# Optimization experiments

Hardware: AMD Instinct MI355X
Metric: run time of the kernel (lower is better)

## Reference

```python
import jax, jax.numpy as jnp
import numpy as np
import math

HEADS = 2
DH = 64
INNER = HEADS * DH  # 128
TOPK = 128
ALPHA = 10.0
N_FREQ = 8  # feature_dim // (2*input_dim) = 64 // 8
OMEGAS = jnp.logspace(1.0, math.log10(128.0), N_FREQ)           # sigma_q = 128
OMEGAS_L = [jnp.logspace(1.0, math.log10(s), N_FREQ) for s in (128.0, 32.0)]
LAYER_NUM = 2


def calc_gamma(grid, omegas):
    # grid: (Q, 4) -> (Q, 4*2*n_freq)
    arg = jnp.pi * grid[:, :, None] * omegas[None, None, :]      # (Q,4,n)
    g = jnp.concatenate([jnp.sin(arg), jnp.cos(arg)], axis=-1)   # (Q,4,2n)
    return g.reshape(grid.shape[0], -1)


def setup_inputs() -> dict:
    key = jax.random.key(0)
    ks = jax.random.split(key, 20)
    B, Q, L, HD, FD, OD = 2, 4096, 1024, 256, 64, 1

    def w(k, shape, fan_in):
        return jax.random.normal(k, shape, dtype=jnp.float32) * (1.0 / np.sqrt(fan_in))

    inp = {
        'x': jax.random.uniform(ks[0], (B, Q, 4), dtype=jnp.float32),
        'tokens': jax.random.normal(ks[1], (B, L, HD), dtype=jnp.float32),
        'query_W': w(ks[2], (FD, HD), FD),
        'query_b': jnp.zeros((HD,), jnp.float32),
        'q_W': w(ks[3], (HD, INNER), HD),
        'kv_W': w(ks[4], (HD, 2 * INNER), HD),
        'out_W': w(ks[5], (INNER, HD), INNER),
        'out_b': jnp.zeros((HD,), jnp.float32),
        'band_W': w(ks[6], (LAYER_NUM, FD, HD), FD),
        'band_b': jnp.zeros((LAYER_NUM, HD), jnp.float32),
        'mod_W': w(ks[7], (LAYER_NUM, HD, HD), HD),
        'mod_b': jnp.zeros((LAYER_NUM, HD), jnp.float32),
        'hv_W': w(ks[8], (LAYER_NUM - 1, HD, HD), HD),
        'hv_b': jnp.zeros((LAYER_NUM - 1, HD), jnp.float32),
        'outl_W': w(ks[9], (LAYER_NUM, HD, OD), HD),
        'outl_b': jnp.zeros((LAYER_NUM, OD), jnp.float32),
        'gD': 8, 'gH': 8, 'gW': 8, 'gT': 8,
    }
    return inp


def reference(x, tokens, query_W, query_b, q_W, kv_W, out_W, out_b,
              band_W, band_b, mod_W, mod_b, hv_W, hv_b, outl_W, outl_b,
              gD, gH, gW, gT):
    B, Q, _ = x.shape
    L = tokens.shape[1]
    grid = x[0]  # (Q, 4) — torch code uses x[0] for all batches

    # --- patch index + approximate relative distances -> sparse attn indices ---
    z_i = (grid[:, 0] * gD).astype(jnp.int32)
    y_i = (grid[:, 1] * gH).astype(jnp.int32)
    x_i = (grid[:, 2] * gW).astype(jnp.int32)
    t_i = (grid[:, 3] * gT).astype(jnp.int32)
    idx = ((t_i * gD + z_i) * gH + y_i) * gW + x_i               # (Q,)
    N = gD * gH * gW * gT
    t = idx / N                                                  # (Q,) float
    tok_pos = (jnp.arange(L, dtype=jnp.float32) + 0.5) / L       # (L,)
    bias = ALPHA * (t[:, None] - tok_pos[None, :]) ** 2          # (Q, L)
    # top-k SMALLEST distances (identical across batch, compute once)
    _, attn_idx = jax.lax.top_k(-bias, TOPK)                     # (Q, k)

    # --- query features ---
    gamma_q = calc_gamma(grid, OMEGAS)                           # (Q, 64)
    x_q = jax.nn.relu(gamma_q @ query_W + query_b)               # (Q, 256)
    x_q = jnp.broadcast_to(x_q[None], (B, Q, x_q.shape[-1]))

    # --- sparse shared-token cross attention ---
    scale = DH ** -0.5
    q = (x_q @ q_W).reshape(B, Q, HEADS, DH)                     # (B,Q,H,Dh)
    kv = tokens @ kv_W                                           # (B,L,2*inner)
    k_full, v_full = kv[..., :INNER], kv[..., INNER:]            # (B,L,inner)
    k_sp = k_full[:, attn_idx, :].reshape(B, Q, TOPK, HEADS, DH)  # (B,Q,k,H,Dh)
    v_sp = v_full[:, attn_idx, :].reshape(B, Q, TOPK, HEADS, DH)
    sim = jnp.einsum('bqhd,bqkhd->bhqk', q, k_sp) * scale        # (B,H,Q,k)
    attn = jax.nn.softmax(sim, axis=-1)
    o = jnp.einsum('bhqk,bqkhd->bqhd', attn, v_sp).reshape(B, Q, INNER)
    modulation = o @ out_W + out_b                               # (B,Q,256)

    # --- per-band modulation ---
    mods = []
    for l in range(LAYER_NUM):
        gamma_l = calc_gamma(grid, OMEGAS_L[l])                  # (Q, 64)
        h_l = jax.nn.relu(gamma_l @ band_W[l] + band_b[l])       # (Q, 256)
        m_l = jax.nn.relu(h_l[None] + modulation @ mod_W[l] + mod_b[l])
        mods.append(m_l)

    h_v = [mods[0]]
    for i in range(LAYER_NUM - 1):
        h_v.append(jax.nn.relu((mods[i + 1] + h_v[i]) @ hv_W[i] + hv_b[i]))

    out = sum(h_v[i] @ outl_W[i] + outl_b[i] for i in range(LAYER_NUM))
    return out  # (B, Q, output_dim)
```

## Files before the change

kernel.cpp:

```cpp
#include <hip/hip_runtime.h>
#include <math.h>

#define BN     2
#define QN     4096
#define LN     1024
#define TOPKN  128
#define PI_F   3.14159265358979323846f

#define LOG2R0 0.52543879f
#define LOG2R1 0.23972456f

#define NCMAX  320
#define PFP    332

typedef __attribute__((ext_vector_type(8))) short  s16x8;
typedef __attribute__((ext_vector_type(4))) short  s16x4;
typedef __attribute__((ext_vector_type(4))) float  f32x4;
typedef unsigned short u16;

__device__ __forceinline__ u16 f2bf(float f) {
    unsigned int u = __float_as_uint(f);
    u = (u + 0x7FFFu + ((u >> 16) & 1u)) >> 16;
    return (u16)u;
}

__device__ __forceinline__ s16x8 ldB(const float* __restrict__ base, int stride) {
    s16x8 r;
    #pragma unroll
    for (int jj = 0; jj < 8; jj++) r[jj] = (short)f2bf(base[(size_t)jj * stride]);
    return r;
}

__device__ __forceinline__ size_t wtile(int n, int k, int K) {
    return (size_t)((n >> 4) * (K >> 5) + (k >> 5)) * 512 + (n & 15) * 32 + (k & 31);
}
__device__ __forceinline__ size_t kidx(int b, int l, int d) {
    return (((size_t)(b * 64 + (l >> 4)) * 16 + (d >> 3)) * 16 + (l & 15)) * 8 + (d & 7);
}
__device__ __forceinline__ size_t vidx(int b, int n, int k) {
    return (((size_t)(b * 8 + (n >> 4)) * 128 + (k >> 3)) * 16 + (n & 15)) * 8 + (k & 7);
}

struct KvS { u16 tok[32 * 264]; };
struct QS  { float shx[128]; u16 gam[32 * 72]; u16 xq[32 * 264]; };
struct TrS { float tile[8][32][33]; };
struct SoS { int hist[1024]; int cur[1024]; };
union PrepS { KvS kv; QS q; TrS tr; SoS so; };

__global__ __launch_bounds__(1024) void prep_kernel(
    const float* __restrict__ tokens, const float* __restrict__ kv_W,
    const float* __restrict__ x, const float* __restrict__ query_W,
    const float* __restrict__ query_b, const float* __restrict__ q_W,
    const float* __restrict__ outW, const float* __restrict__ bandW,
    const float* __restrict__ modW, const float* __restrict__ hvW,
    const int* __restrict__ gDp, const int* __restrict__ gHp,
    const int* __restrict__ gWp, const int* __restrict__ gTp,
    u16* __restrict__ qall, u16* __restrict__ kbf, u16* __restrict__ vtbf,
    u16* __restrict__ outT, u16* __restrict__ bandT,
    u16* __restrict__ modT, u16* __restrict__ hvT,
    int* __restrict__ perm, int* __restrict__ ssort)
{
    __shared__ __align__(16) PrepS sm;
    const int bid = blockIdx.x;
    const int t   = threadIdx.x;
    const int wid = t >> 6, lane = t & 63;
    const int quad = lane >> 4, l16 = lane & 15;

    if (bid < 64) {
        int l0 = bid * 32;
        int b = l0 >> 10, lloc = l0 & 1023;
        #pragma unroll
        for (int i = 0; i < 8; i++) {
            int idx = i * 1024 + t; int row = idx >> 8, col = idx & 255;
            sm.kv.tok[row * 264 + col] = f2bf(tokens[(size_t)(l0 + row) * 256 + col]);
        }
        __syncthreads();
        int m0 = (wid & 1) * 16;
        int c0 = (wid >> 1) * 32;
        f32x4 acc[2];
        acc[0] = (f32x4){0.f, 0.f, 0.f, 0.f};
        acc[1] = (f32x4){0.f, 0.f, 0.f, 0.f};
        for (int kc = 0; kc < 8; kc++) {
            s16x8 a = *(const s16x8*)&sm.kv.tok[(m0 + l16) * 264 + kc * 32 + quad * 8];
            #pragma unroll
            for (int sub = 0; sub < 2; sub++) {
                s16x8 bfr = ldB(&kv_W[(size_t)(kc * 32 + quad * 8) * 256 + c0 + sub * 16 + l16], 256);
                acc[sub] = __builtin_amdgcn_mfma_f32_16x16x32_bf16(a, bfr, acc[sub], 0, 0, 0);
            }
        }
        #pragma unroll
        for (int sub = 0; sub < 2; sub++) {
            int col = c0 + sub * 16 + l16;
            if (col < 128) {
                #pragma unroll
                for (int r = 0; r < 4; r++)
                    kbf[kidx(b, lloc + m0 + quad * 4 + r, col)] = f2bf(acc[sub][r]);
            } else {
                s16x4 pk;
                pk[0] = (short)f2bf(acc[sub][0]); pk[1] = (short)f2bf(acc[sub][1]);
                pk[2] = (short)f2bf(acc[sub][2]); pk[3] = (short)f2bf(acc[sub][3]);
                *(s16x4*)&vtbf[vidx(b, col - 128, lloc + m0 + quad * 4)] = pk;
            }
        }
    } else if (bid < 192) {
        int p0 = (bid - 64) * 32;
        if (t < 128) sm.q.shx[t] = x[p0 * 4 + t];
        __syncthreads();
        #pragma unroll
        for (int j = 0; j < 2; j++) {
            int e = t * 2 + j;
            int g = e >> 6, f = e & 63;
            int c = f >> 4, jj = f & 15, oi = jj & 7;
            float om = 10.0f * exp2f((float)oi * LOG2R0);
            float arg = PI_F * sm.q.shx[g * 4 + c] * om;
            sm.q.gam[g * 72 + f] = f2bf((jj < 8) ? __sinf(arg) : __cosf(arg));
        }
        __syncthreads();
        int m0 = (wid & 1) * 16;
        {
            int c0 = (wid >> 1) * 32;
            f32x4 acc[2];
            acc[0] = (f32x4){0.f, 0.f, 0.f, 0.f};
            acc[1] = (f32x4){0.f, 0.f, 0.f, 0.f};
            for (int kc = 0; kc < 2; kc++) {
                s16x8 a = *(const s16x8*)&sm.q.gam[(m0 + l16) * 72 + kc * 32 + quad * 8];
                #pragma unroll
                for (int sub = 0; sub < 2; sub++) {
                    s16x8 bfr = ldB(&query_W[(size_t)(kc * 32 + quad * 8) * 256 + c0 + sub * 16 + l16], 256);
                    acc[sub] = __builtin_amdgcn_mfma_f32_16x16x32_bf16(a, bfr, acc[sub], 0, 0, 0);
                }
            }
            #pragma unroll
            for (int sub = 0; sub < 2; sub++) {
                int col = c0 + sub * 16 + l16;
                float bias = query_b[col];
                #pragma unroll
                for (int r = 0; r < 4; r++)
                    sm.q.xq[(m0 + quad * 4 + r) * 264 + col] = f2bf(fmaxf(acc[sub][r] + bias, 0.f));
            }
        }
        __syncthreads();
        {
            int n0q = (wid >> 1) * 16;
            f32x4 acc2 = (f32x4){0.f, 0.f, 0.f, 0.f};
            for (int kc = 0; kc < 8; kc++) {
                s16x8 a = *(const s16x8*)&sm.q.xq[(m0 + l16) * 264 + kc * 32 + quad * 8];
                s16x8 bfr = ldB(&q_W[(size_t)(kc * 32 + quad * 8) * 128 + n0q + l16], 128);
                acc2 = __builtin_amdgcn_mfma_f32_16x16x32_bf16(a, bfr, acc2, 0, 0, 0);
            }
            #pragma unroll
            for (int r = 0; r < 4; r++)
                qall[(size_t)(p0 + m0 + quad * 4 + r) * 128 + n0q + l16] = f2bf(acc2[r]);
        }
    } else if (bid < 224) {
        int base = (bid - 192) * 8;
        int tx = t & 31, ty = (t >> 5) & 31;
        #pragma unroll
        for (int it = 0; it < 8; it++) {
            int lt_g = base + it;
            const float* src; int K, lt;
            if (lt_g < 32)       { src = outW;  K = 128; lt = lt_g; }
            else if (lt_g < 64)  { src = bandW; K = 128; lt = lt_g - 32; }
            else if (lt_g < 192) { src = modW;  K = 512; lt = lt_g - 64; }
            else                 { src = hvW;   K = 256; lt = lt_g - 192; }
            int tk = K >> 5;
            int k0 = (lt % tk) * 32, n0 = (lt / tk) * 32;
            sm.tr.tile[it][ty][tx] = src[(size_t)(k0 + ty) * 256 + n0 + tx];
        }
        __syncthreads();
        #pragma unroll
        for (int it = 0; it < 8; it++) {
            int lt_g = base + it;
            u16* dst; int K, lt;
            if (lt_g < 32)       { dst = outT;  K = 128; lt = lt_g; }
            else if (lt_g < 64)  { dst = bandT; K = 128; lt = lt_g - 32; }
            else if (lt_g < 192) { dst = modT;  K = 512; lt = lt_g - 64; }
            else                 { dst = hvT;   K = 256; lt = lt_g - 192; }
            int tk = K >> 5;
            int k0 = (lt % tk) * 32, n0 = (lt / tk) * 32;
            dst[wtile(n0 + ty, k0 + tx, K)] = f2bf(sm.tr.tile[it][tx][ty]);
        }
    } else {
        int gD = gDp[0], gH = gHp[0], gW = gWp[0], gT = gTp[0];
        int Ng = gD * gH * gW * gT;
        sm.so.hist[t] = 0;
        __syncthreads();
        int sarr[4];
        #pragma unroll
        for (int i = 0; i < 4; i++) {
            int q = i * 1024 + t;
            float4 xv = *(const float4*)&x[q * 4];
            int zi = (int)(xv.x * (float)gD);
            int yi = (int)(xv.y * (float)gH);
            int xi = (int)(xv.z * (float)gW);
            int ti = (int)(xv.w * (float)gT);
            int idx = ((ti * gD + zi) * gH + yi) * gW + xi;
            float tt = (float)idx / (float)Ng;
            int s = (int)ceilf(tt * (float)LN - ((float)(TOPKN / 2) + 0.5f));
            s = min(max(s, 0), LN - TOPKN);
            sarr[i] = s;
            atomicAdd(&sm.so.hist[s], 1);
        }
        __syncthreads();
        int cnt = sm.so.hist[t];
        int incl = cnt;
        #pragma unroll
        for (int off = 1; off < 64; off <<= 1) {
            int u = __shfl_up(incl, off);
            if (lane >= off) incl += u;
        }
        if (lane == 63) sm.so.cur[wid] = incl;
        __syncthreads();
        if (wid == 0) {
            int v = (lane < 16) ? sm.so.cur[lane] : 0;
            #pragma unroll
            for (int off = 1; off < 16; off <<= 1) {
                int u = __shfl_up(v, off);
                if (lane >= off) v += u;
            }
            if (lane < 16) sm.so.cur[lane] = v;
        }
        __syncthreads();
        int woff = wid ? sm.so.cur[wid - 1] : 0;
        sm.so.hist[t] = woff + incl - cnt;
        __syncthreads();
        #pragma unroll
        for (int i = 0; i < 4; i++) {
            int q = i * 1024 + t;
            int pos = atomicAdd(&sm.so.hist[sarr[i]], 1);
            perm[pos] = q;
            ssort[pos] = sarr[i];
        }
    }
}

__global__ __launch_bounds__(1024, 8) void fused_kernel(
    const float* __restrict__ x,
    const u16* __restrict__ kbf, const u16* __restrict__ vtbf,
    const u16* __restrict__ qall,
    const int* __restrict__ perm, const int* __restrict__ ssort,
    const u16* __restrict__ outT, const float* __restrict__ out_b,
    const u16* __restrict__ bandT, const float* __restrict__ band_b,
    const u16* __restrict__ modT, const float* __restrict__ mod_b,
    const u16* __restrict__ hvT, const float* __restrict__ hv_b,
    const float* __restrict__ outl_W, const float* __restrict__ outl_b,
    float* __restrict__ out)
{
    const int bid = blockIdx.x;
    const int b   = bid >> 8;
    const int sp0 = (bid & 255) * 16;
    const int t   = threadIdx.x;
    const int wid = t >> 6, lane = t & 63;
    const int quad = lane >> 4, l16 = lane & 15;

    __shared__ __align__(16) u16 q_bf[16 * 136];
    __shared__ __align__(16) u16 gam_lds[32 * 72];
    __shared__ __align__(16) float scores32[32 * PFP];
    __shared__ __align__(16) u16 o_lds[16 * 136];
    __shared__ float fin[256];
    __shared__ float sh_xc[64];
    __shared__ int sh_pq[16], sh_s[16];

    u16* modu_lds = (u16*)scores32;
    u16* s01_lds  = ((u16*)scores32) + 16 * 264;

    if (t < 16) { sh_pq[t] = perm[sp0 + t]; sh_s[t] = ssort[sp0 + t]; }
    __syncthreads();

    {
        int m = t >> 6, d = (t & 63) * 2;
        *(unsigned int*)&q_bf[m * 136 + d] =
            *(const unsigned int*)&qall[(size_t)sh_pq[m] * 128 + d];
    }
    if (t < 64) sh_xc[t] = x[(size_t)sh_pq[t >> 2] * 4 + (t & 3)];
    __syncthreads();

    #pragma unroll
    for (int j = 0; j < 2; j++) {
        int e = t * 2 + j;
        int l = e >> 10, g = (e >> 6) & 15, f = e & 63;
        int c = f >> 4, jj = f & 15, oi = jj & 7;
        float om = 10.0f * exp2f((float)oi * (l ? LOG2R1 : LOG2R0));
        float arg = PI_F * sh_xc[g * 4 + c] * om;
        gam_lds[(l * 16 + g) * 72 + f] = f2bf((jj < 8) ? __sinf(arg) : __cosf(arg));
    }

    const int u0    = sh_s[0] & ~15;
    const int ncols = min((sh_s[15] + 128 - u0 + 31) & ~31, NCMAX);
    const int nsub  = ncols >> 4;

    {
        s16x8 aq00 = *(const s16x8*)&q_bf[l16 * 136 + quad * 8];
        s16x8 aq01 = *(const s16x8*)&q_bf[l16 * 136 + 32 + quad * 8];
        s16x8 aq10 = *(const s16x8*)&q_bf[l16 * 136 + 64 + quad * 8];
        s16x8 aq11 = *(const s16x8*)&q_bf[l16 * 136 + 96 + quad * 8];
        for (int j = wid; j < 2 * nsub; j += 16) {
            int h = (j >= nsub) ? 1 : 0;
            int sub = j - h * nsub;
            int lrow = u0 + sub * 16 + l16;
            f32x4 acc = (f32x4){0.f, 0.f, 0.f, 0.f};
            s16x8 b0 = *(const s16x8*)&kbf[kidx(b, lrow, h * 64 + quad * 8)];
            s16x8 b1 = *(const s16x8*)&kbf[kidx(b, lrow, h * 64 + 32 + quad * 8)];
            acc = __builtin_amdgcn_mfma_f32_16x16x32_bf16(h ? aq10 : aq00, b0, acc, 0, 0, 0);
            acc = __builtin_amdgcn_mfma_f32_16x16x32_bf16(h ? aq11 : aq01, b1, acc, 0, 0, 0);
            #pragma unroll
            for (int r = 0; r < 4; r++)
                scores32[(h * 16 + quad * 4 + r) * PFP + sub * 16 + l16] = acc[r];
        }
    }
    __syncthreads();

    {
        int g = wid;
        int sg = sh_s[g];
        #pragma unroll
        for (int rr = 0; rr < 2; rr++) {
            int row = g + rr * 16;
            float vals[5]; int ok[5];
            float mx = -1e30f;
            #pragma unroll
            for (int i = 0; i < 5; i++) {
                int c = lane + 64 * i;
                float v = scores32[row * PFP + c] * 0.125f;
                int key = u0 + c;
                int o2 = (c < ncols) && (key >= sg) && (key < sg + 128);
                vals[i] = v; ok[i] = o2;
                if (o2) mx = fmaxf(mx, v);
            }
            #pragma unroll
            for (int off = 1; off < 64; off <<= 1) mx = fmaxf(mx, __shfl_xor(mx, off));
            float sum = 0.f, e5[5];
            #pragma unroll
            for (int i = 0; i < 5; i++) {
                float e = ok[i] ? __expf(vals[i] - mx) : 0.f;
                e5[i] = e; sum += e;
            }
            #pragma unroll
            for (int off = 1; off < 64; off <<= 1) sum += __shfl_xor(sum, off);
            float inv = 1.f / sum;
            u16* prow = (u16*)&scores32[row * PFP];
            #pragma unroll
            for (int i = 0; i < 5; i++) {
                int c = lane + 64 * i;
                prow[c] = f2bf(e5[i] * inv);
            }
        }
    }
    __syncthreads();

    if (wid < 8) {
        int n0 = wid * 16;
        int hh = n0 >> 6;
        const u16* prow = (const u16*)&scores32[(hh * 16 + l16) * PFP];
        f32x4 acc = (f32x4){0.f, 0.f, 0.f, 0.f};
        for (int kc = 0; kc < (NCMAX >> 5); kc++) {
            s16x8 a = *(const s16x8*)&prow[kc * 32 + quad * 8];
            int koff = u0 + kc * 32 + quad * 8;
            koff = min(koff, 1016);
            s16x8 bfr = *(const s16x8*)&vtbf[vidx(b, n0 + l16, koff)];
            acc = __builtin_amdgcn_mfma_f32_16x16x32_bf16(a, bfr, acc, 0, 0, 0);
        }
        #pragma unroll
        for (int r = 0; r < 4; r++)
            o_lds[(quad * 4 + r) * 136 + n0 + l16] = f2bf(acc[r]);
    }
    __syncthreads();

    const int n0 = wid * 16;
    float m0f[4];

    {
        f32x4 acc = (f32x4){0.f, 0.f, 0.f, 0.f};
        #pragma unroll
        for (int kc = 0; kc < 4; kc++) {
            s16x8 a = *(const s16x8*)&o_lds[l16 * 136 + kc * 32 + quad * 8];
            s16x8 bfr = *(const s16x8*)&outT[wtile(n0 + l16, kc * 32 + quad * 8, 128)];
            acc = __builtin_amdgcn_mfma_f32_16x16x32_bf16(a, bfr, acc, 0, 0, 0);
        }
        int col = n0 + l16;
        float bias = out_b[col];
        #pragma unroll
        for (int r = 0; r < 4; r++)
            modu_lds[(quad * 4 + r) * 264 + col] = f2bf(acc[r] + bias);
    }
    __syncthreads();

    #pragma unroll
    for (int l = 0; l < 2; l++) {
        f32x4 acc1 = (f32x4){0.f, 0.f, 0.f, 0.f};
        f32x4 acc2 = (f32x4){0.f, 0.f, 0.f, 0.f};
        #pragma unroll
        for (int kc = 0; kc < 2; kc++) {
            s16x8 a = *(const s16x8*)&gam_lds[(l * 16 + l16) * 72 + kc * 32 + quad * 8];
            s16x8 bfr = *(const s16x8*)&bandT[wtile(n0 + l16, l * 64 + kc * 32 + quad * 8, 128)];
            acc1 = __builtin_amdgcn_mfma_f32_16x16x32_bf16(a, bfr, acc1, 0, 0, 0);
        }
        #pragma unroll
        for (int kc = 0; kc < 8; kc++) {
            s16x8 a = *(const s16x8*)&modu_lds[l16 * 264 + kc * 32 + quad * 8];
            s16x8 bfr = *(const s16x8*)&modT[wtile(n0 + l16, l * 256 + kc * 32 + quad * 8, 512)];
            acc2 = __builtin_amdgcn_mfma_f32_16x16x32_bf16(a, bfr, acc2, 0, 0, 0);
        }
        int col = n0 + l16;
        float bb = band_b[l * 256 + col];
        float mb = mod_b[l * 256 + col];
        #pragma unroll
        for (int r = 0; r < 4; r++) {
            float hval = fmaxf(acc1[r] + bb, 0.f);
            float mval = fmaxf(hval + acc2[r] + mb, 0.f);
            if (l == 0) m0f[r] = mval;
            else s01_lds[(quad * 4 + r) * 264 + col] = f2bf(m0f[r] + mval);
        }
    }
    __syncthreads();

    {
        f32x4 acc = (f32x4){0.f, 0.f, 0.f, 0.f};
        #pragma unroll
        for (int kc = 0; kc < 8; kc++) {
            s16x8 a = *(const s16x8*)&s01_lds[l16 * 264 + kc * 32 + quad * 8];
            s16x8 bfr = *(const s16x8*)&hvT[wtile(n0 + l16, kc * 32 + quad * 8, 256)];
            acc = __builtin_amdgcn_mfma_f32_16x16x32_bf16(a, bfr, acc, 0, 0, 0);
        }
        int col = n0 + l16;
        float w0 = outl_W[col], w1 = outl_W[256 + col], hb = hv_b[col];
        #pragma unroll
        for (int r = 0; r < 4; r++) {
            float hvv = fmaxf(acc[r] + hb, 0.f);
            float pv = m0f[r] * w0 + hvv * w1;
            #pragma unroll
            for (int off = 1; off < 16; off <<= 1) pv += __shfl_xor(pv, off);
            if (l16 == 0) fin[wid * 16 + quad * 4 + r] = pv;
        }
    }
    __syncthreads();
    if (t < 16) {
        float s2 = outl_b[0] + outl_b[1];
        #pragma unroll
        for (int w = 0; w < 16; w++) s2 += fin[w * 16 + t];
        out[(size_t)b * QN + sh_pq[t]] = s2;
    }
}

extern "C" void kernel_launch(void* const* d_in, const int* in_sizes, int n_in,
                              void* d_out, int out_size, void* d_ws, size_t ws_size,
                              hipStream_t stream)
{
    const float* x       = (const float*)d_in[0];
    const float* tokens  = (const float*)d_in[1];
    const float* query_W = (const float*)d_in[2];
    const float* query_b = (const float*)d_in[3];
    const float* q_W     = (const float*)d_in[4];
    const float* kv_W    = (const float*)d_in[5];
    const float* out_W   = (const float*)d_in[6];
    const float* out_b   = (const float*)d_in[7];
    const float* band_W  = (const float*)d_in[8];
    const float* band_b  = (const float*)d_in[9];
    const float* mod_W   = (const float*)d_in[10];
    const float* mod_b   = (const float*)d_in[11];
    const float* hv_W    = (const float*)d_in[12];
    const float* hv_b    = (const float*)d_in[13];
    const float* outl_W  = (const float*)d_in[14];
    const float* outl_b  = (const float*)d_in[15];
    const int*   gD      = (const int*)d_in[16];
    const int*   gH      = (const int*)d_in[17];
    const int*   gW      = (const int*)d_in[18];
    const int*   gT      = (const int*)d_in[19];

    float* ws   = (float*)d_ws;
    u16* qall   = (u16*)ws;
    u16* wb = (u16*)(ws + 524288);
    u16* kbf   = wb;
    u16* vtbf  = wb + 262144;
    u16* outT  = wb + 524288;
    u16* bandT = wb + 557056;
    u16* modT  = wb + 589824;
    u16* hvT   = wb + 720896;
    int* perm  = (int*)(wb + 786432);
    int* ssort = perm + 4096;
    float* out = (float*)d_out;

    prep_kernel<<<225, 1024, 0, stream>>>(tokens, kv_W, x, query_W, query_b, q_W,
                                          out_W, band_W, mod_W, hv_W,
                                          gD, gH, gW, gT,
                                          qall, kbf, vtbf, outT, bandT, modT, hvT,
                                          perm, ssort);
    fused_kernel<<<512, 1024, 0, stream>>>(x, kbf, vtbf, qall, perm, ssort,
        outT, out_b, bandT, band_b, modT, mod_b, hvT, hv_b,
        outl_W, outl_b, out);
}
```

Baseline: 125.0 us.

## Process 32 queries per block to reuse weight fragments across two row tiles

Each fused block now handles 32 sorted queries instead of 16, halving the grid to 256 blocks. Every weight B-fragment loaded from global memory feeds two MFMAs (one per 16-row half), roughly halving weight and K/V fetch traffic per query. The PV loop now iterates only over the actual column count, and the score buffer grows to cover a wider key window. The cost is double the LDS use and fewer blocks, only 256 for the 256 CUs, which lowers occupancy and latency hiding. Keys beyond the wider window are clipped more often if the sorted queries spread further.

```diff
diff --git a/kernel.cpp b/kernel.cpp
--- a/kernel.cpp
+++ b/kernel.cpp
@@ -10,8 +10,8 @@
 #define LOG2R0 0.52543879f
 #define LOG2R1 0.23972456f
 
-#define NCMAX  320
-#define PFP    332
+#define NCMAX  384
+#define PFP    388
 
 typedef __attribute__((ext_vector_type(8))) short  s16x8;
 typedef __attribute__((ext_vector_type(4))) short  s16x4;
@@ -234,7 +234,7 @@
     }
 }
 
-__global__ __launch_bounds__(1024, 8) void fused_kernel(
+__global__ __launch_bounds__(1024, 4) void fused_kernel(
     const float* __restrict__ x,
     const u16* __restrict__ kbf, const u16* __restrict__ vtbf,
     const u16* __restrict__ qall,
@@ -247,79 +247,86 @@
     float* __restrict__ out)
 {
     const int bid = blockIdx.x;
-    const int b   = bid >> 8;
-    const int sp0 = (bid & 255) * 16;
+    const int b   = bid >> 7;
+    const int g0  = (bid & 127) * 32;
     const int t   = threadIdx.x;
     const int wid = t >> 6, lane = t & 63;
     const int quad = lane >> 4, l16 = lane & 15;
 
-    __shared__ __align__(16) u16 q_bf[16 * 136];
-    __shared__ __align__(16) u16 gam_lds[32 * 72];
-    __shared__ __align__(16) float scores32[32 * PFP];
-    __shared__ __align__(16) u16 o_lds[16 * 136];
-    __shared__ float fin[256];
-    __shared__ float sh_xc[64];
-    __shared__ int sh_pq[16], sh_s[16];
+    __shared__ __align__(16) u16 q_bf[32 * 136];
+    __shared__ __align__(16) u16 gam_lds[64 * 72];
+    __shared__ __align__(16) float scores32[64 * PFP];
+    __shared__ __align__(16) u16 o_lds[32 * 136];
+    __shared__ float fin[16 * 32];
+    __shared__ float sh_xc[128];
+    __shared__ int sh_pq[32], sh_s[32];
 
     u16* modu_lds = (u16*)scores32;
-    u16* s01_lds  = ((u16*)scores32) + 16 * 264;
-
-    if (t < 16) { sh_pq[t] = perm[sp0 + t]; sh_s[t] = ssort[sp0 + t]; }
+    u16* s01_lds  = ((u16*)scores32) + 32 * 264;
+
+    if (t < 32) { sh_pq[t] = perm[g0 + t]; sh_s[t] = ssort[g0 + t]; }
     __syncthreads();
 
     {
-        int m = t >> 6, d = (t & 63) * 2;
-        *(unsigned int*)&q_bf[m * 136 + d] =
-            *(const unsigned int*)&qall[(size_t)sh_pq[m] * 128 + d];
-    }
-    if (t < 64) sh_xc[t] = x[(size_t)sh_pq[t >> 2] * 4 + (t & 3)];
+        int m = t >> 5, d = (t & 31) * 4;
+        *(uint2*)&q_bf[m * 136 + d] = *(const uint2*)&qall[(size_t)sh_pq[m] * 128 + d];
+    }
+    if (t < 128) sh_xc[t] = x[(size_t)sh_pq[t >> 2] * 4 + (t & 3)];
     __syncthreads();
 
     #pragma unroll
-    for (int j = 0; j < 2; j++) {
-        int e = t * 2 + j;
-        int l = e >> 10, g = (e >> 6) & 15, f = e & 63;
+    for (int j = 0; j < 4; j++) {
+        int e = j * 1024 + t;
+        int l = e >> 11, g = (e >> 6) & 31, f = e & 63;
         int c = f >> 4, jj = f & 15, oi = jj & 7;
         float om = 10.0f * exp2f((float)oi * (l ? LOG2R1 : LOG2R0));
         float arg = PI_F * sh_xc[g * 4 + c] * om;
-        gam_lds[(l * 16 + g) * 72 + f] = f2bf((jj < 8) ? __sinf(arg) : __cosf(arg));
+        gam_lds[(l * 32 + g) * 72 + f] = f2bf((jj < 8) ? __sinf(arg) : __cosf(arg));
     }
 
     const int u0    = sh_s[0] & ~15;
-    const int ncols = min((sh_s[15] + 128 - u0 + 31) & ~31, NCMAX);
+    const int ncols = min((sh_s[31] + 128 - u0 + 31) & ~31, NCMAX);
     const int nsub  = ncols >> 4;
+    const int nkc   = ncols >> 5;
 
     {
-        s16x8 aq00 = *(const s16x8*)&q_bf[l16 * 136 + quad * 8];
-        s16x8 aq01 = *(const s16x8*)&q_bf[l16 * 136 + 32 + quad * 8];
-        s16x8 aq10 = *(const s16x8*)&q_bf[l16 * 136 + 64 + quad * 8];
-        s16x8 aq11 = *(const s16x8*)&q_bf[l16 * 136 + 96 + quad * 8];
+        s16x8 aq[2][4];
+        #pragma unroll
+        for (int rh = 0; rh < 2; rh++)
+            #pragma unroll
+            for (int c = 0; c < 4; c++)
+                aq[rh][c] = *(const s16x8*)&q_bf[(rh * 16 + l16) * 136 + c * 32 + quad * 8];
         for (int j = wid; j < 2 * nsub; j += 16) {
             int h = (j >= nsub) ? 1 : 0;
             int sub = j - h * nsub;
             int lrow = u0 + sub * 16 + l16;
-            f32x4 acc = (f32x4){0.f, 0.f, 0.f, 0.f};
+            f32x4 acc0 = (f32x4){0.f, 0.f, 0.f, 0.f};
+            f32x4 acc1 = (f32x4){0.f, 0.f, 0.f, 0.f};
             s16x8 b0 = *(const s16x8*)&kbf[kidx(b, lrow, h * 64 + quad * 8)];
             s16x8 b1 = *(const s16x8*)&kbf[kidx(b, lrow, h * 64 + 32 + quad * 8)];
-            acc = __builtin_amdgcn_mfma_f32_16x16x32_bf16(h ? aq10 : aq00, b0, acc, 0, 0, 0);
-            acc = __builtin_amdgcn_mfma_f32_16x16x32_bf16(h ? aq11 : aq01, b1, acc, 0, 0, 0);
-            #pragma unroll
-            for (int r = 0; r < 4; r++)
-                scores32[(h * 16 + quad * 4 + r) * PFP + sub * 16 + l16] = acc[r];
+            acc0 = __builtin_amdgcn_mfma_f32_16x16x32_bf16(aq[0][h * 2 + 0], b0, acc0, 0, 0, 0);
+            acc0 = __builtin_amdgcn_mfma_f32_16x16x32_bf16(aq[0][h * 2 + 1], b1, acc0, 0, 0, 0);
+            acc1 = __builtin_amdgcn_mfma_f32_16x16x32_bf16(aq[1][h * 2 + 0], b0, acc1, 0, 0, 0);
+            acc1 = __builtin_amdgcn_mfma_f32_16x16x32_bf16(aq[1][h * 2 + 1], b1, acc1, 0, 0, 0);
+            #pragma unroll
+            for (int r = 0; r < 4; r++) {
+                scores32[(h * 32 + quad * 4 + r) * PFP + sub * 16 + l16] = acc0[r];
+                scores32[(h * 32 + 16 + quad * 4 + r) * PFP + sub * 16 + l16] = acc1[r];
+            }
         }
     }
     __syncthreads();
 
     {
-        int g = wid;
-        int sg = sh_s[g];
-        #pragma unroll
-        for (int rr = 0; rr < 2; rr++) {
-            int row = g + rr * 16;
-            float vals[5]; int ok[5];
+        #pragma unroll
+        for (int rr = 0; rr < 4; rr++) {
+            int row = wid + rr * 16;
+            int qq  = row & 31;
+            int sg  = sh_s[qq];
+            float vals[6]; int ok[6];
             float mx = -1e30f;
             #pragma unroll
-            for (int i = 0; i < 5; i++) {
+            for (int i = 0; i < 6; i++) {
                 int c = lane + 64 * i;
                 float v = scores32[row * PFP + c] * 0.125f;
                 int key = u0 + c;
@@ -329,115 +336,141 @@
             }
             #pragma unroll
             for (int off = 1; off < 64; off <<= 1) mx = fmaxf(mx, __shfl_xor(mx, off));
-            float sum = 0.f, e5[5];
-            #pragma unroll
-            for (int i = 0; i < 5; i++) {
+            float sum = 0.f, e6[6];
+            #pragma unroll
+            for (int i = 0; i < 6; i++) {
                 float e = ok[i] ? __expf(vals[i] - mx) : 0.f;
-                e5[i] = e; sum += e;
+                e6[i] = e; sum += e;
             }
             #pragma unroll
             for (int off = 1; off < 64; off <<= 1) sum += __shfl_xor(sum, off);
             float inv = 1.f / sum;
             u16* prow = (u16*)&scores32[row * PFP];
             #pragma unroll
-            for (int i = 0; i < 5; i++) {
+            for (int i = 0; i < 6; i++) {
                 int c = lane + 64 * i;
-                prow[c] = f2bf(e5[i] * inv);
-            }
-        }
-    }
-    __syncthreads();
-
-    if (wid < 8) {
-        int n0 = wid * 16;
-        int hh = n0 >> 6;
-        const u16* prow = (const u16*)&scores32[(hh * 16 + l16) * PFP];
+                if (c < ncols) prow[c] = f2bf(e6[i] * inv);
+            }
+        }
+    }
+    __syncthreads();
+
+    {
+        int ct = wid & 7, rh = wid >> 3;
+        int h = ct >> 2;
+        const u16* prow = (const u16*)&scores32[(h * 32 + rh * 16 + l16) * PFP];
         f32x4 acc = (f32x4){0.f, 0.f, 0.f, 0.f};
-        for (int kc = 0; kc < (NCMAX >> 5); kc++) {
+        #pragma unroll 2
+        for (int kc = 0; kc < nkc; kc++) {
             s16x8 a = *(const s16x8*)&prow[kc * 32 + quad * 8];
             int koff = u0 + kc * 32 + quad * 8;
             koff = min(koff, 1016);
-            s16x8 bfr = *(const s16x8*)&vtbf[vidx(b, n0 + l16, koff)];
+            s16x8 bfr = *(const s16x8*)&vtbf[vidx(b, ct * 16 + l16, koff)];
             acc = __builtin_amdgcn_mfma_f32_16x16x32_bf16(a, bfr, acc, 0, 0, 0);
         }
         #pragma unroll
         for (int r = 0; r < 4; r++)
-            o_lds[(quad * 4 + r) * 136 + n0 + l16] = f2bf(acc[r]);
+            o_lds[(rh * 16 + quad * 4 + r) * 136 + ct * 16 + l16] = f2bf(acc[r]);
     }
     __syncthreads();
 
     const int n0 = wid * 16;
-    float m0f[4];
+    float m0f[2][4];
 
     {
-        f32x4 acc = (f32x4){0.f, 0.f, 0.f, 0.f};
+        f32x4 am0 = (f32x4){0.f, 0.f, 0.f, 0.f};
+        f32x4 am1 = (f32x4){0.f, 0.f, 0.f, 0.f};
         #pragma unroll
         for (int kc = 0; kc < 4; kc++) {
-            s16x8 a = *(const s16x8*)&o_lds[l16 * 136 + kc * 32 + quad * 8];
             s16x8 bfr = *(const s16x8*)&outT[wtile(n0 + l16, kc * 32 + quad * 8, 128)];
-            acc = __builtin_amdgcn_mfma_f32_16x16x32_bf16(a, bfr, acc, 0, 0, 0);
+            s16x8 a0 = *(const s16x8*)&o_lds[l16 * 136 + kc * 32 + quad * 8];
+            s16x8 a1 = *(const s16x8*)&o_lds[(16 + l16) * 136 + kc * 32 + quad * 8];
+            am0 = __builtin_amdgcn_mfma_f32_16x16x32_bf16(a0, bfr, am0, 0, 0, 0);
+            am1 = __builtin_amdgcn_mfma_f32_16x16x32_bf16(a1, bfr, am1, 0, 0, 0);
         }
         int col = n0 + l16;
         float bias = out_b[col];
         #pragma unroll
-        for (int r = 0; r < 4; r++)
-            modu_lds[(quad * 4 + r) * 264 + col] = f2bf(acc[r] + bias);
+        for (int r = 0; r < 4; r++) {
+            modu_lds[(quad * 4 + r) * 264 + col] = f2bf(am0[r] + bias);
+            modu_lds[(16 + quad * 4 + r) * 264 + col] = f2bf(am1[r] + bias);
+        }
     }
     __syncthreads();
 
     #pragma unroll
     for (int l = 0; l < 2; l++) {
-        f32x4 acc1 = (f32x4){0.f, 0.f, 0.f, 0.f};
-        f32x4 acc2 = (f32x4){0.f, 0.f, 0.f, 0.f};
+        f32x4 ab0 = (f32x4){0.f, 0.f, 0.f, 0.f};
+        f32x4 ab1 = (f32x4){0.f, 0.f, 0.f, 0.f};
+        f32x4 am0 = (f32x4){0.f, 0.f, 0.f, 0.f};
+        f32x4 am1 = (f32x4){0.f, 0.f, 0.f, 0.f};
         #pragma unroll
         for (int kc = 0; kc < 2; kc++) {
-            s16x8 a = *(const s16x8*)&gam_lds[(l * 16 + l16) * 72 + kc * 32 + quad * 8];
             s16x8 bfr = *(const s16x8*)&bandT[wtile(n0 + l16, l * 64 + kc * 32 + quad * 8, 128)];
-            acc1 = __builtin_amdgcn_mfma_f32_16x16x32_bf16(a, bfr, acc1, 0, 0, 0);
+            s16x8 a0 = *(const s16x8*)&gam_lds[(l * 32 + l16) * 72 + kc * 32 + quad * 8];
+            s16x8 a1 = *(const s16x8*)&gam_lds[(l * 32 + 16 + l16) * 72 + kc * 32 + quad * 8];
+            ab0 = __builtin_amdgcn_mfma_f32_16x16x32_bf16(a0, bfr, ab0, 0, 0, 0);
+            ab1 = __builtin_amdgcn_mfma_f32_16x16x32_bf16(a1, bfr, ab1, 0, 0, 0);
         }
         #pragma unroll
         for (int kc = 0; kc < 8; kc++) {
-            s16x8 a = *(const s16x8*)&modu_lds[l16 * 264 + kc * 32 + quad * 8];
             s16x8 bfr = *(const s16x8*)&modT[wtile(n0 + l16, l * 256 + kc * 32 + quad * 8, 512)];
-            acc2 = __builtin_amdgcn_mfma_f32_16x16x32_bf16(a, bfr, acc2, 0, 0, 0);
+            s16x8 a0 = *(const s16x8*)&modu_lds[l16 * 264 + kc * 32 + quad * 8];
+            s16x8 a1 = *(const s16x8*)&modu_lds[(16 + l16) * 264 + kc * 32 + quad * 8];
+            am0 = __builtin_amdgcn_mfma_f32_16x16x32_bf16(a0, bfr, am0, 0, 0, 0);
+            am1 = __builtin_amdgcn_mfma_f32_16x16x32_bf16(a1, bfr, am1, 0, 0, 0);
         }
         int col = n0 + l16;
         float bb = band_b[l * 256 + col];
         float mb = mod_b[l * 256 + col];
         #pragma unroll
         for (int r = 0; r < 4; r++) {
-            float hval = fmaxf(acc1[r] + bb, 0.f);
-            float mval = fmaxf(hval + acc2[r] + mb, 0.f);
-            if (l == 0) m0f[r] = mval;
-            else s01_lds[(quad * 4 + r) * 264 + col] = f2bf(m0f[r] + mval);
+            float h0 = fmaxf(ab0[r] + bb, 0.f);
+            float v0 = fmaxf(h0 + am0[r] + mb, 0.f);
+            float h1 = fmaxf(ab1[r] + bb, 0.f);
+            float v1 = fmaxf(h1 + am1[r] + mb, 0.f);
+            if (l == 0) { m0f[0][r] = v0; m0f[1][r] = v1; }
+            else {
+                s01_lds[(quad * 4 + r) * 264 + col] = f2bf(m0f[0][r] + v0);
+                s01_lds[(16 + quad * 4 + r) * 264 + col] = f2bf(m0f[1][r] + v1);
+            }
         }
     }
     __syncthreads();
 
     {
-        f32x4 acc = (f32x4){0.f, 0.f, 0.f, 0.f};
+        f32x4 ah0 = (f32x4){0.f, 0.f, 0.f, 0.f};
+        f32x4 ah1 = (f32x4){0.f, 0.f, 0.f, 0.f};
         #pragma unroll
         for (int kc = 0; kc < 8; kc++) {
-            s16x8 a = *(const s16x8*)&s01_lds[l16 * 264 + kc * 32 + quad * 8];
             s16x8 bfr = *(const s16x8*)&hvT[wtile(n0 + l16, kc * 32 + quad * 8, 256)];
-            acc = __builtin_amdgcn_mfma_f32_16x16x32_bf16(a, bfr, acc, 0, 0, 0);
+            s16x8 a0 = *(const s16x8*)&s01_lds[l16 * 264 + kc * 32 + quad * 8];
+            s16x8 a1 = *(const s16x8*)&s01_lds[(16 + l16) * 264 + kc * 32 + quad * 8];
+            ah0 = __builtin_amdgcn_mfma_f32_16x16x32_bf16(a0, bfr, ah0, 0, 0, 0);
+            ah1 = __builtin_amdgcn_mfma_f32_16x16x32_bf16(a1, bfr, ah1, 0, 0, 0);
         }
         int col = n0 + l16;
         float w0 = outl_W[col], w1 = outl_W[256 + col], hb = hv_b[col];
         #pragma unroll
         for (int r = 0; r < 4; r++) {
-            float hvv = fmaxf(acc[r] + hb, 0.f);
-            float pv = m0f[r] * w0 + hvv * w1;
-            #pragma unroll
-            for (int off = 1; off < 16; off <<= 1) pv += __shfl_xor(pv, off);
-            if (l16 == 0) fin[wid * 16 + quad * 4 + r] = pv;
-        }
-    }
-    __syncthreads();
-    if (t < 16) {
+            float pv0 = m0f[0][r] * w0 + fmaxf(ah0[r] + hb, 0.f) * w1;
+            float pv1 = m0f[1][r] * w0 + fmaxf(ah1[r] + hb, 0.f) * w1;
+            #pragma unroll
+            for (int off = 1; off < 16; off <<= 1) {
+                pv0 += __shfl_xor(pv0, off);
+                pv1 += __shfl_xor(pv1, off);
+            }
+            if (l16 == 0) {
+                fin[wid * 32 + quad * 4 + r] = pv0;
+                fin[wid * 32 + 16 + quad * 4 + r] = pv1;
+            }
+        }
+    }
+    __syncthreads();
+    if (t < 32) {
         float s2 = outl_b[0] + outl_b[1];
         #pragma unroll
-        for (int w = 0; w < 16; w++) s2 += fin[w * 16 + t];
+        for (int w = 0; w < 16; w++) s2 += fin[w * 32 + t];
         out[(size_t)b * QN + sh_pq[t]] = s2;
     }
 }
@@ -485,7 +518,7 @@
                                           gD, gH, gW, gT,
                                           qall, kbf, vtbf, outT, bandT, modT, hvT,
                                           perm, ssort);
-    fused_kernel<<<512, 1024, 0, stream>>>(x, kbf, vtbf, qall, perm, ssort,
+    fused_kernel<<<256, 1024, 0, stream>>>(x, kbf, vtbf, qall, perm, ssort,
         outT, out_b, bandT, band_b, modT, mod_b, hvT, hv_b,
         outl_W, outl_b, out);
 }
```

Measured after the change: 121.6 us. -2.7%, faster.
